# Optimization experiments

Hardware: AMD Instinct MI355X
Metric: run time of the kernel (lower is better)

The kernel has to match this reference:

```python
import jax, jax.numpy as jnp
import numpy as np

B, D_IN, H, D_OUT = 1024, 512, 512, 512


def _act(v):
    # torch.relu(x) ** 2
    r = jnp.maximum(v, 0.0)
    return r * r


def setup_inputs() -> dict:
    key = jax.random.key(0)
    ks = jax.random.split(key, 8)
    x = jax.random.normal(ks[0], (B, D_IN), dtype=jnp.float32)
    # input_to_hidden: Linear(D_IN, H)
    W_in = jax.random.normal(ks[1], (D_IN, H), dtype=jnp.float32) / np.sqrt(D_IN)
    b_in = jax.random.normal(ks[2], (H,), dtype=jnp.float32) * 0.01
    # hidden_to_hidden[i]: Linear(1, H-i-1). Pack into padded arrays [H-1, H]
    # where row i, column j is the weight feeding output index j (valid only j > i).
    W_hh = jax.random.normal(ks[3], (H - 1, H), dtype=jnp.float32) * 0.02
    b_hh = jax.random.normal(ks[4], (H - 1, H), dtype=jnp.float32) * 0.01
    # hidden_to_output: Linear(H, D_OUT)
    W_out = jax.random.normal(ks[5], (H, D_OUT), dtype=jnp.float32) / np.sqrt(H)
    b_out = jax.random.normal(ks[6], (D_OUT,), dtype=jnp.float32) * 0.01
    return {"x": x, "W_in": W_in, "b_in": b_in, "W_hh": W_hh, "b_hh": b_hh,
            "W_out": W_out, "b_out": b_out}


def reference(x, W_in, b_in, W_hh, b_hh, W_out, b_out):
    h0 = _act(x @ W_in + b_in)  # [B, H]
    hid = h0.shape[1]
    col = jnp.arange(hid)

    def step(h, inp):
        i, w, b = inp  # w, b: [H] padded rows
        src = jnp.take(h, i, axis=1)  # [B], uses UPDATED h (strict sequential dep)
        contrib = _act(src[:, None] * w[None, :] + b[None, :])  # [B, H]
        mask = (col > i).astype(h.dtype)  # only columns i+1.. get updated
        return h + contrib * mask[None, :], None

    xs = (jnp.arange(hid - 1), W_hh, b_hh)
    h, _ = jax.lax.scan(step, h0, xs)
    return h @ W_out + b_out  # [B, D_OUT]
```

## Files before the change

### kernel.cpp

```cpp
#include <hip/hip_runtime.h>

#define B_SZ 1024
#define DIN 512
#define HH 512
#define DOUT 512

typedef short bf16x8 __attribute__((ext_vector_type(8)));
typedef float f32x4 __attribute__((ext_vector_type(4)));

__device__ __forceinline__ unsigned short f2bf(float f) {
    unsigned int u = __float_as_uint(f);
    u += 0x7FFFu + ((u >> 16) & 1u);
    return (unsigned short)(u >> 16);
}
__device__ __forceinline__ float bf2f(unsigned short s) {
    return __uint_as_float(((unsigned int)s) << 16);
}

__device__ __forceinline__ uint4 cvt8(const float4& a0, const float4& a1, int term) {
    const float av[8] = {a0.x, a0.y, a0.z, a0.w, a1.x, a1.y, a1.z, a1.w};
    unsigned int p[4];
    #pragma unroll
    for (int q = 0; q < 4; ++q) {
        float f0 = av[2 * q], f1 = av[2 * q + 1];
        unsigned short h0 = f2bf(f0), h1 = f2bf(f1);
        if (term == 1) { h0 = f2bf(f0 - bf2f(h0)); h1 = f2bf(f1 - bf2f(h1)); }
        p[q] = (unsigned int)h0 | ((unsigned int)h1 << 16);
    }
    uint4 v; v.x = p[0]; v.y = p[1]; v.z = p[2]; v.w = p[3];
    return v;
}

__device__ __forceinline__ void gload_lds16(const void* g, void* l) {
    __builtin_amdgcn_global_load_lds(
        (__attribute__((address_space(1))) void*)g,
        (__attribute__((address_space(3))) void*)l, 16, 0, 0);
}

__device__ __forceinline__ void convW_body(const float* __restrict__ W,
                                           uint4* __restrict__ dst, int t) {
    const int lane = t & 63;
    const int fb   = t >> 6;
    const int ks   = fb >> 5;
    const int nf   = fb & 31;
    const int col  = nf * 16 + (lane & 15);
    const int kb   = ks * 32 + ((lane >> 4) << 3);
    const int term = kb >> 9;
    const int c0   = kb & 511;
    unsigned short o[8];
    #pragma unroll
    for (int j = 0; j < 8; ++j) {
        const float f = W[(size_t)(c0 + j) * 512 + col];
        unsigned short hi = f2bf(f);
        o[j] = (term == 2) ? f2bf(f - bf2f(hi)) : hi;
    }
    uint4 v;
    v.x = (unsigned int)o[0] | ((unsigned int)o[1] << 16);
    v.y = (unsigned int)o[2] | ((unsigned int)o[3] << 16);
    v.z = (unsigned int)o[4] | ((unsigned int)o[5] << 16);
    v.w = (unsigned int)o[6] | ((unsigned int)o[7] << 16);
    dst[t] = v;
}

template <int C>
__device__ __forceinline__ void pack_bulk(const float* __restrict__ W_hh,
                                          const float* __restrict__ b_hh,
                                          float2* __restrict__ wbk, int e) {
    constexpr int NK = 7 - C;
    constexpr int CB = (C==0?0:C==1?7:C==2?13:C==3?18:C==4?22:C==5?25:27) * 4096;
    const int s   = e / (NK * 64);
    const int rem = e - s * (NK * 64);
    const int row = 64 * C + s;
    const int col = 64 * (C + 1) + rem;
    float2 o;
    o.x = W_hh[(size_t)row * 512 + col];
    o.y = b_hh[(size_t)row * 512 + col];
    wbk[CB + e] = o;
}

__global__ __launch_bounds__(256)
void prep_all(const float* __restrict__ W_hh, const float* __restrict__ b_hh,
              float2* __restrict__ wdg, float2* __restrict__ wbk,
              const float* __restrict__ W_in, uint4* __restrict__ Bin,
              const float* __restrict__ W_out, uint4* __restrict__ Bout) {
    const int b = blockIdx.x;
    const int tid = threadIdx.x;
    if (b < 128) {
        const int idx = b * 256 + tid;
        const int i = idx >> 6, l = idx & 63;
        float2 o;
        if (i < 511 && l > (i & 63)) {
            const int col = ((i >> 6) << 6) + l;
            o.x = W_hh[(size_t)i * 512 + col];
            o.y = b_hh[(size_t)i * 512 + col];
        } else { o.x = 0.0f; o.y = -1.0f; }
        wdg[idx] = o;
    } else if (b < 576) {
        const int rb = b - 128;
        if      (rb < 112) pack_bulk<0>(W_hh, b_hh, wbk, (rb      ) * 256 + tid);
        else if (rb < 208) pack_bulk<1>(W_hh, b_hh, wbk, (rb - 112) * 256 + tid);
        else if (rb < 288) pack_bulk<2>(W_hh, b_hh, wbk, (rb - 208) * 256 + tid);
        else if (rb < 352) pack_bulk<3>(W_hh, b_hh, wbk, (rb - 288) * 256 + tid);
        else if (rb < 400) pack_bulk<4>(W_hh, b_hh, wbk, (rb - 352) * 256 + tid);
        else if (rb < 432) pack_bulk<5>(W_hh, b_hh, wbk, (rb - 400) * 256 + tid);
        else               pack_bulk<6>(W_hh, b_hh, wbk, (rb - 432) * 256 + tid);
    } else if (b < 960) {
        convW_body(W_in, Bin, (b - 576) * 256 + tid);
    } else {
        convW_body(W_out, Bout, (b - 960) * 256 + tid);
    }
}

template <bool ACT>
__global__ __launch_bounds__(512, 2)
void mfma_gemm(const float* __restrict__ A,
               const uint4* __restrict__ Bg,
               const float* __restrict__ bias,
               float* __restrict__ C) {
    __shared__ uint4 lds[2][768];
    const int tid  = threadIdx.x;
    const int lane = tid & 63;
    const int w    = tid >> 6;
    const int mfw  = w & 3;
    const int nfw  = w >> 2;
    const int mf0  = blockIdx.x * 4;
    const int nf0  = blockIdx.y * 2;

    const int ks_s = tid >> 8;
    const int mf_s = (tid >> 6) & 3;
    const int arow = (mf0 + mf_s) * 16 + (lane & 15);
    const int koff = (lane >> 4) << 3;
    const int bks  = tid >> 7;
    const int bnf  = (tid >> 6) & 1;

    float4 Ra0, Ra1; uint4 R2;
    auto stage = [&](int s) {
        const int kp = (s * 2 + ks_s) * 32 + koff;
        const int c  = kp & 511;
        Ra0 = *(const float4*)&A[(size_t)arow * 512 + c];
        Ra1 = *(const float4*)&A[(size_t)arow * 512 + c + 4];
        if (tid < 256)
            R2 = Bg[(size_t)((s * 2 + bks) * 32 + nf0 + bnf) * 64 + lane];
    };
    auto write_tile = [&](int buf, int s) {
        const int kp = (s * 2 + ks_s) * 32 + koff;
        lds[buf][ks_s * 256 + mf_s * 64 + lane] = cvt8(Ra0, Ra1, kp >> 9);
        if (tid < 256)
            lds[buf][512 + bks * 128 + bnf * 64 + lane] = R2;
    };

    f32x4 acc = {0.f, 0.f, 0.f, 0.f};

    stage(0);
    write_tile(0, 0);
    stage(1);
    __syncthreads();

    for (int s = 0; s < 24; ++s) {
        const int cur = s & 1;
        if (s + 1 < 24) write_tile(cur ^ 1, s + 1);
        if (s + 2 < 24) stage(s + 2);
        __builtin_amdgcn_sched_barrier(0);

        bf16x8 aF0 = *(const bf16x8*)&lds[cur][          mfw * 64 + lane];
        bf16x8 aF1 = *(const bf16x8*)&lds[cur][256     + mfw * 64 + lane];
        bf16x8 bF0 = *(const bf16x8*)&lds[cur][512     + nfw * 64 + lane];
        bf16x8 bF1 = *(const bf16x8*)&lds[cur][512+128 + nfw * 64 + lane];
        acc = __builtin_amdgcn_mfma_f32_16x16x32_bf16(aF0, bF0, acc, 0, 0, 0);
        acc = __builtin_amdgcn_mfma_f32_16x16x32_bf16(aF1, bF1, acc, 0, 0, 0);
        __syncthreads();
    }

    const int colg  = (nf0 + nfw) * 16 + (lane & 15);
    const float bv  = bias[colg];
    const int rbase = (mf0 + mfw) * 16 + ((lane >> 4) << 2);
    #pragma unroll
    for (int r = 0; r < 4; ++r) {
        float v = acc[r] + bv;
        if (ACT) { v = fmaxf(v, 0.f); v = v * v; }
        C[(size_t)(rbase + r) * 512 + colg] = v;
    }
}

template <int C>
__device__ __forceinline__ void scan_chunk(const float2* __restrict__ wdg,
                                           const float2* __restrict__ wbk,
                                           float2 (* __restrict__ smb)[3584],
                                           float hr[8], int lane, int tid) {
    constexpr int NK = 7 - C;
    constexpr int CB = (C==0?0:C==1?7:C==2?13:C==3?18:C==4?22:C==5?25:C==6?27:27) * 4096;
    const float2* dptr = wdg + (64 * C) * 64 + lane;

    float2 Wd[16];
    #pragma unroll
    for (int q = 0; q < 16; ++q) Wd[q] = dptr[q * 64];

    const char* gch = (const char*)(wbk + CB);
    char* lbase = (char*)(&smb[0][0]) + ((tid >> 6) << 10);
    auto stage = [&](int t, int buf) {
        const char* g = gch + (size_t)t * (NK * 4096);
        char* l = lbase + buf * 28672;
        #pragma unroll
        for (int u = 0; u < NK; ++u)
            gload_lds16(g + (size_t)((u << 8) + tid) * 16, l + (u << 12));
    };
    if constexpr (NK > 0) stage(0, 0);

    for (int t = 0; t < 4; ++t) {
        #pragma unroll
        for (int q = 0; q < 16; ++q) {
            const int s = t * 16 + q;
            if (!(C == 7 && s == 63)) {
                const float hi = __uint_as_float(
                    __builtin_amdgcn_readlane(__float_as_uint(hr[C]), s));
                const float tv = fmaf(hi, Wd[q].x, Wd[q].y);
                const float rv = fmaxf(tv, 0.f);
                hr[C] = fmaf(rv, rv, hr[C]);
            }
            if (t < 3) Wd[q] = dptr[(s + 16) * 64];
        }
    }

    if constexpr (NK > 0) {
        __syncthreads();
        for (int t = 0; t < 8; ++t) {
            const int buf = t & 1;
            if (t + 1 < 8) stage(t + 1, buf ^ 1);
            __builtin_amdgcn_sched_barrier(0);

            #pragma unroll 2
            for (int s = 0; s < 8; ++s) {
                const float hi = __uint_as_float(
                    __builtin_amdgcn_readlane(__float_as_uint(hr[C]), t * 8 + s));
                #pragma unroll
                for (int k = 0; k < NK; ++k) {
                    const float2 wv = smb[buf][(s * NK + k) * 64 + lane];
                    const float tv = fmaf(hi, wv.x, wv.y);
                    const float rv = fmaxf(tv, 0.f);
                    hr[C + 1 + k] = fmaf(rv, rv, hr[C + 1 + k]);
                }
            }
            __syncthreads();
        }
    }
}

__global__ __launch_bounds__(256, 1)
void scan_kernel(const float2* __restrict__ wdg, const float2* __restrict__ wbk,
                 float* __restrict__ h) {
    __shared__ __align__(16) float2 smb[2][3584];
    const int tid  = threadIdx.x;
    const int lane = tid & 63;
    const int wave = tid >> 6;
    const int row  = blockIdx.x * 4 + wave;
    float* hrow = h + (size_t)row * HH;

    float hr[8];
    #pragma unroll
    for (int k = 0; k < 8; ++k) hr[k] = hrow[lane + 64 * k];

    scan_chunk<0>(wdg, wbk, smb, hr, lane, tid);
    scan_chunk<1>(wdg, wbk, smb, hr, lane, tid);
    scan_chunk<2>(wdg, wbk, smb, hr, lane, tid);
    scan_chunk<3>(wdg, wbk, smb, hr, lane, tid);
    scan_chunk<4>(wdg, wbk, smb, hr, lane, tid);
    scan_chunk<5>(wdg, wbk, smb, hr, lane, tid);
    scan_chunk<6>(wdg, wbk, smb, hr, lane, tid);
    scan_chunk<7>(wdg, wbk, smb, hr, lane, tid);

    #pragma unroll
    for (int k = 0; k < 8; ++k) hrow[lane + 64 * k] = hr[k];
}

extern "C" void kernel_launch(void* const* d_in, const int* in_sizes, int n_in,
                              void* d_out, int out_size, void* d_ws, size_t ws_size,
                              hipStream_t stream) {
    const float* x     = (const float*)d_in[0];
    const float* W_in  = (const float*)d_in[1];
    const float* b_in  = (const float*)d_in[2];
    const float* W_hh  = (const float*)d_in[3];
    const float* b_hh  = (const float*)d_in[4];
    const float* W_out = (const float*)d_in[5];
    const float* b_out = (const float*)d_in[6];
    float* out = (float*)d_out;

    char* ws = (char*)d_ws;
    float2* wdg  = (float2*)ws;
    float2* wbk  = (float2*)(ws + 0x040000u);
    float*  h    = (float*)(ws + 0x120000u);
    uint4*  Bin  = (uint4*)(ws + 0x320000u);
    uint4*  Bout = (uint4*)(ws + 0x4A0000u);

    prep_all<<<dim3(1344), dim3(256), 0, stream>>>(W_hh, b_hh, wdg, wbk,
                                                   W_in, Bin, W_out, Bout);

    mfma_gemm<true><<<dim3(16, 16), dim3(512), 0, stream>>>(x, Bin, b_in, h);

    scan_kernel<<<dim3(256), dim3(256), 0, stream>>>(wdg, wbk, h);

    mfma_gemm<false><<<dim3(16, 16), dim3(512), 0, stream>>>(h, Bout, b_out, out);
}
```

Before: 157.1 us.

## Split each scan row across two waves with LDS partial-sum exchange

Each batch row is now handled by two waves instead of one, doubling the grid to 512 blocks with 2 rows per block. The waves split the off-diagonal source steps by parity and accumulate partial sums that are combined through shared memory before each diagonal chunk, which one wave still computes alone. Launch bounds are raised to allow two blocks per CU. This adds parallelism to the latency-bound sequential scan, at the cost of extra barriers, idle time for the second wave during the diagonal part, and twice the staged weight traffic per row.

```diff
diff --git a/kernel.cpp b/kernel.cpp
--- a/kernel.cpp
+++ b/kernel.cpp
@@ -186,14 +186,11 @@
 __device__ __forceinline__ void scan_chunk(const float2* __restrict__ wdg,
                                            const float2* __restrict__ wbk,
                                            float2 (* __restrict__ smb)[3584],
-                                           float hr[8], int lane, int tid) {
+                                           float (* __restrict__ comm)[64],
+                                           float hrp[8], int lane, int row_l,
+                                           int par, int tid) {
     constexpr int NK = 7 - C;
     constexpr int CB = (C==0?0:C==1?7:C==2?13:C==3?18:C==4?22:C==5?25:C==6?27:27) * 4096;
-    const float2* dptr = wdg + (64 * C) * 64 + lane;
-
-    float2 Wd[16];
-    #pragma unroll
-    for (int q = 0; q < 16; ++q) Wd[q] = dptr[q * 64];
 
     const char* gch = (const char*)(wbk + CB);
     char* lbase = (char*)(&smb[0][0]) + ((tid >> 6) << 10);
@@ -205,39 +202,53 @@
             gload_lds16(g + (size_t)((u << 8) + tid) * 16, l + (u << 12));
     };
     if constexpr (NK > 0) stage(0, 0);
-
-    for (int t = 0; t < 4; ++t) {
+    __builtin_amdgcn_sched_barrier(0);
+
+    if (par == 1) comm[row_l][lane] = hrp[C];
+    __syncthreads();
+
+    if (par == 0) {
+        hrp[C] += comm[row_l][lane];
+        const float2* dptr = wdg + (64 * C) * 64 + lane;
+        float2 Wd[16];
         #pragma unroll
-        for (int q = 0; q < 16; ++q) {
-            const int s = t * 16 + q;
-            if (!(C == 7 && s == 63)) {
-                const float hi = __uint_as_float(
-                    __builtin_amdgcn_readlane(__float_as_uint(hr[C]), s));
-                const float tv = fmaf(hi, Wd[q].x, Wd[q].y);
-                const float rv = fmaxf(tv, 0.f);
-                hr[C] = fmaf(rv, rv, hr[C]);
+        for (int q = 0; q < 16; ++q) Wd[q] = dptr[q * 64];
+        for (int t = 0; t < 4; ++t) {
+            #pragma unroll
+            for (int q = 0; q < 16; ++q) {
+                const int s = t * 16 + q;
+                if (!(C == 7 && s == 63)) {
+                    const float hi = __uint_as_float(
+                        __builtin_amdgcn_readlane(__float_as_uint(hrp[C]), s));
+                    const float tv = fmaf(hi, Wd[q].x, Wd[q].y);
+                    const float rv = fmaxf(tv, 0.f);
+                    hrp[C] = fmaf(rv, rv, hrp[C]);
+                }
+                if (t < 3) Wd[q] = dptr[(s + 16) * 64];
             }
-            if (t < 3) Wd[q] = dptr[(s + 16) * 64];
         }
-    }
+        comm[row_l][lane] = hrp[C];
+    }
+    __syncthreads();
 
     if constexpr (NK > 0) {
-        __syncthreads();
+        const float hsrc = (par == 0) ? hrp[C] : comm[row_l][lane];
         for (int t = 0; t < 8; ++t) {
             const int buf = t & 1;
             if (t + 1 < 8) stage(t + 1, buf ^ 1);
             __builtin_amdgcn_sched_barrier(0);
 
-            #pragma unroll 2
-            for (int s = 0; s < 8; ++s) {
+            #pragma unroll
+            for (int sl = 0; sl < 4; ++sl) {
+                const int srow = 2 * sl + par;
                 const float hi = __uint_as_float(
-                    __builtin_amdgcn_readlane(__float_as_uint(hr[C]), t * 8 + s));
+                    __builtin_amdgcn_readlane(__float_as_uint(hsrc), t * 8 + srow));
                 #pragma unroll
                 for (int k = 0; k < NK; ++k) {
-                    const float2 wv = smb[buf][(s * NK + k) * 64 + lane];
+                    const float2 wv = smb[buf][(srow * NK + k) * 64 + lane];
                     const float tv = fmaf(hi, wv.x, wv.y);
                     const float rv = fmaxf(tv, 0.f);
-                    hr[C + 1 + k] = fmaf(rv, rv, hr[C + 1 + k]);
+                    hrp[C + 1 + k] = fmaf(rv, rv, hrp[C + 1 + k]);
                 }
             }
             __syncthreads();
@@ -245,31 +256,35 @@
     }
 }
 
-__global__ __launch_bounds__(256, 1)
+__global__ __launch_bounds__(256, 2)
 void scan_kernel(const float2* __restrict__ wdg, const float2* __restrict__ wbk,
                  float* __restrict__ h) {
     __shared__ __align__(16) float2 smb[2][3584];
-    const int tid  = threadIdx.x;
-    const int lane = tid & 63;
-    const int wave = tid >> 6;
-    const int row  = blockIdx.x * 4 + wave;
-    float* hrow = h + (size_t)row * HH;
-
-    float hr[8];
+    __shared__ float comm[2][64];
+    const int tid   = threadIdx.x;
+    const int lane  = tid & 63;
+    const int w     = tid >> 6;
+    const int row_l = w & 1;
+    const int par   = w >> 1;
+    float* hrow = h + (size_t)(blockIdx.x * 2 + row_l) * HH;
+
+    float hrp[8];
     #pragma unroll
-    for (int k = 0; k < 8; ++k) hr[k] = hrow[lane + 64 * k];
-
-    scan_chunk<0>(wdg, wbk, smb, hr, lane, tid);
-    scan_chunk<1>(wdg, wbk, smb, hr, lane, tid);
-    scan_chunk<2>(wdg, wbk, smb, hr, lane, tid);
-    scan_chunk<3>(wdg, wbk, smb, hr, lane, tid);
-    scan_chunk<4>(wdg, wbk, smb, hr, lane, tid);
-    scan_chunk<5>(wdg, wbk, smb, hr, lane, tid);
-    scan_chunk<6>(wdg, wbk, smb, hr, lane, tid);
-    scan_chunk<7>(wdg, wbk, smb, hr, lane, tid);
-
-    #pragma unroll
-    for (int k = 0; k < 8; ++k) hrow[lane + 64 * k] = hr[k];
+    for (int k = 0; k < 8; ++k) hrp[k] = (par == 0) ? hrow[lane + 64 * k] : 0.f;
+
+    scan_chunk<0>(wdg, wbk, smb, comm, hrp, lane, row_l, par, tid);
+    scan_chunk<1>(wdg, wbk, smb, comm, hrp, lane, row_l, par, tid);
+    scan_chunk<2>(wdg, wbk, smb, comm, hrp, lane, row_l, par, tid);
+    scan_chunk<3>(wdg, wbk, smb, comm, hrp, lane, row_l, par, tid);
+    scan_chunk<4>(wdg, wbk, smb, comm, hrp, lane, row_l, par, tid);
+    scan_chunk<5>(wdg, wbk, smb, comm, hrp, lane, row_l, par, tid);
+    scan_chunk<6>(wdg, wbk, smb, comm, hrp, lane, row_l, par, tid);
+    scan_chunk<7>(wdg, wbk, smb, comm, hrp, lane, row_l, par, tid);
+
+    if (par == 0) {
+        #pragma unroll
+        for (int k = 0; k < 8; ++k) hrow[lane + 64 * k] = hrp[k];
+    }
 }
 
 extern "C" void kernel_launch(void* const* d_in, const int* in_sizes, int n_in,
@@ -296,7 +311,7 @@
 
     mfma_gemm<true><<<dim3(16, 16), dim3(512), 0, stream>>>(x, Bin, b_in, h);
 
-    scan_kernel<<<dim3(256), dim3(256), 0, stream>>>(wdg, wbk, h);
+    scan_kernel<<<dim3(512), dim3(256), 0, stream>>>(wdg, wbk, h);
 
     mfma_gemm<false><<<dim3(16, 16), dim3(512), 0, stream>>>(h, Bout, b_out, out);
 }
```

Measured after the change: 151.1 us. 3.8% less time.

## Split scan rows across waves with partial-sum reduction for more parallelism

Applied to the files above, without the earlier changes.

Changes the scan kernel from one batch row per wave to two rows per block, with each of the four waves handling a quarter of the source steps in the off-diagonal update and keeping partial sums. Before each diagonal chunk, the partial sums are reduced through shared memory, and the designated wave runs the serial diagonal recurrence. The grid is doubled to 512 blocks and launch bounds allow two blocks per CU. The aim is to shorten the per-row serial critical path and raise occupancy. In exchange it adds extra barriers, LDS traffic for the reductions, and idle waves during the diagonal phase.

```diff
diff --git a/kernel.cpp b/kernel.cpp
--- a/kernel.cpp
+++ b/kernel.cpp
@@ -36,6 +36,7 @@
         (__attribute__((address_space(1))) void*)g,
         (__attribute__((address_space(3))) void*)l, 16, 0, 0);
 }
+__device__ __forceinline__ void SB() { __builtin_amdgcn_sched_barrier(0); }
 
 __device__ __forceinline__ void convW_body(const float* __restrict__ W,
                                            uint4* __restrict__ dst, int t) {
@@ -186,14 +187,11 @@
 __device__ __forceinline__ void scan_chunk(const float2* __restrict__ wdg,
                                            const float2* __restrict__ wbk,
                                            float2 (* __restrict__ smb)[3584],
-                                           float hr[8], int lane, int tid) {
+                                           float (* __restrict__ comm)[4][64],
+                                           float hA[8], float hB[8],
+                                           int lane, int p, int tid) {
     constexpr int NK = 7 - C;
     constexpr int CB = (C==0?0:C==1?7:C==2?13:C==3?18:C==4?22:C==5?25:C==6?27:27) * 4096;
-    const float2* dptr = wdg + (64 * C) * 64 + lane;
-
-    float2 Wd[16];
-    #pragma unroll
-    for (int q = 0; q < 16; ++q) Wd[q] = dptr[q * 64];
 
     const char* gch = (const char*)(wbk + CB);
     char* lbase = (char*)(&smb[0][0]) + ((tid >> 6) << 10);
@@ -205,39 +203,68 @@
             gload_lds16(g + (size_t)((u << 8) + tid) * 16, l + (u << 12));
     };
     if constexpr (NK > 0) stage(0, 0);
-
-    for (int t = 0; t < 4; ++t) {
+    SB();
+
+    if (p != 0) comm[0][p][lane] = hA[C];
+    if (p != 1) comm[1][p][lane] = hB[C];
+    __syncthreads();
+
+    auto diag = [&](float& x) {
+        const float2* dptr = wdg + (64 * C) * 64 + lane;
+        float2 Wd[16];
         #pragma unroll
-        for (int q = 0; q < 16; ++q) {
-            const int s = t * 16 + q;
-            if (!(C == 7 && s == 63)) {
-                const float hi = __uint_as_float(
-                    __builtin_amdgcn_readlane(__float_as_uint(hr[C]), s));
-                const float tv = fmaf(hi, Wd[q].x, Wd[q].y);
-                const float rv = fmaxf(tv, 0.f);
-                hr[C] = fmaf(rv, rv, hr[C]);
+        for (int q = 0; q < 16; ++q) Wd[q] = dptr[q * 64];
+        for (int t = 0; t < 4; ++t) {
+            #pragma unroll
+            for (int q = 0; q < 16; ++q) {
+                const int s = t * 16 + q;
+                if (!(C == 7 && s == 63)) {
+                    const float hi = __uint_as_float(
+                        __builtin_amdgcn_readlane(__float_as_uint(x), s));
+                    const float tv = fmaf(hi, Wd[q].x, Wd[q].y);
+                    const float rv = fmaxf(tv, 0.f);
+                    x = fmaf(rv, rv, x);
+                }
+                if (t < 3) Wd[q] = dptr[(s + 16) * 64];
             }
-            if (t < 3) Wd[q] = dptr[(s + 16) * 64];
         }
-    }
+    };
+    if (p == 0) {
+        hA[C] += comm[0][1][lane] + comm[0][2][lane] + comm[0][3][lane];
+        diag(hA[C]);
+        comm[0][0][lane] = hA[C];
+    } else if (p == 1) {
+        hB[C] += comm[1][0][lane] + comm[1][2][lane] + comm[1][3][lane];
+        diag(hB[C]);
+        comm[1][1][lane] = hB[C];
+    }
+    __syncthreads();
 
     if constexpr (NK > 0) {
-        __syncthreads();
+        const float hsA = (p == 0) ? hA[C] : comm[0][0][lane];
+        const float hsB = (p == 1) ? hB[C] : comm[1][1][lane];
         for (int t = 0; t < 8; ++t) {
             const int buf = t & 1;
             if (t + 1 < 8) stage(t + 1, buf ^ 1);
-            __builtin_amdgcn_sched_barrier(0);
-
-            #pragma unroll 2
-            for (int s = 0; s < 8; ++s) {
-                const float hi = __uint_as_float(
-                    __builtin_amdgcn_readlane(__float_as_uint(hr[C]), t * 8 + s));
+            SB();
+
+            #pragma unroll
+            for (int sl = 0; sl < 2; ++sl) {
+                const int srow = p + 4 * sl;
+                const int s = t * 8 + srow;
+                const float hiA = __uint_as_float(
+                    __builtin_amdgcn_readlane(__float_as_uint(hsA), s));
+                const float hiB = __uint_as_float(
+                    __builtin_amdgcn_readlane(__float_as_uint(hsB), s));
                 #pragma unroll
                 for (int k = 0; k < NK; ++k) {
-                    const float2 wv = smb[buf][(s * NK + k) * 64 + lane];
-                    const float tv = fmaf(hi, wv.x, wv.y);
-                    const float rv = fmaxf(tv, 0.f);
-                    hr[C + 1 + k] = fmaf(rv, rv, hr[C + 1 + k]);
+                    const float2 wv = smb[buf][(srow * NK + k) * 64 + lane];
+                    float tv = fmaf(hiA, wv.x, wv.y);
+                    float rv = fmaxf(tv, 0.f);
+                    hA[C + 1 + k] = fmaf(rv, rv, hA[C + 1 + k]);
+                    tv = fmaf(hiB, wv.x, wv.y);
+                    rv = fmaxf(tv, 0.f);
+                    hB[C + 1 + k] = fmaf(rv, rv, hB[C + 1 + k]);
                 }
             }
             __syncthreads();
@@ -245,31 +272,40 @@
     }
 }
 
-__global__ __launch_bounds__(256, 1)
+__global__ __launch_bounds__(256, 2)
 void scan_kernel(const float2* __restrict__ wdg, const float2* __restrict__ wbk,
                  float* __restrict__ h) {
     __shared__ __align__(16) float2 smb[2][3584];
+    __shared__ float comm[2][4][64];
     const int tid  = threadIdx.x;
     const int lane = tid & 63;
-    const int wave = tid >> 6;
-    const int row  = blockIdx.x * 4 + wave;
-    float* hrow = h + (size_t)row * HH;
-
-    float hr[8];
+    const int p    = tid >> 6;
+    float* hrowA = h + (size_t)(blockIdx.x * 2    ) * HH;
+    float* hrowB = h + (size_t)(blockIdx.x * 2 + 1) * HH;
+
+    float hA[8], hB[8];
     #pragma unroll
-    for (int k = 0; k < 8; ++k) hr[k] = hrow[lane + 64 * k];
-
-    scan_chunk<0>(wdg, wbk, smb, hr, lane, tid);
-    scan_chunk<1>(wdg, wbk, smb, hr, lane, tid);
-    scan_chunk<2>(wdg, wbk, smb, hr, lane, tid);
-    scan_chunk<3>(wdg, wbk, smb, hr, lane, tid);
-    scan_chunk<4>(wdg, wbk, smb, hr, lane, tid);
-    scan_chunk<5>(wdg, wbk, smb, hr, lane, tid);
-    scan_chunk<6>(wdg, wbk, smb, hr, lane, tid);
-    scan_chunk<7>(wdg, wbk, smb, hr, lane, tid);
-
-    #pragma unroll
-    for (int k = 0; k < 8; ++k) hrow[lane + 64 * k] = hr[k];
+    for (int k = 0; k < 8; ++k) {
+        hA[k] = (p == 0) ? hrowA[lane + 64 * k] : 0.f;
+        hB[k] = (p == 1) ? hrowB[lane + 64 * k] : 0.f;
+    }
+
+    scan_chunk<0>(wdg, wbk, smb, comm, hA, hB, lane, p, tid);
+    scan_chunk<1>(wdg, wbk, smb, comm, hA, hB, lane, p, tid);
+    scan_chunk<2>(wdg, wbk, smb, comm, hA, hB, lane, p, tid);
+    scan_chunk<3>(wdg, wbk, smb, comm, hA, hB, lane, p, tid);
+    scan_chunk<4>(wdg, wbk, smb, comm, hA, hB, lane, p, tid);
+    scan_chunk<5>(wdg, wbk, smb, comm, hA, hB, lane, p, tid);
+    scan_chunk<6>(wdg, wbk, smb, comm, hA, hB, lane, p, tid);
+    scan_chunk<7>(wdg, wbk, smb, comm, hA, hB, lane, p, tid);
+
+    if (p == 0) {
+        #pragma unroll
+        for (int k = 0; k < 8; ++k) hrowA[lane + 64 * k] = hA[k];
+    } else if (p == 1) {
+        #pragma unroll
+        for (int k = 0; k < 8; ++k) hrowB[lane + 64 * k] = hB[k];
+    }
 }
 
 extern "C" void kernel_launch(void* const* d_in, const int* in_sizes, int n_in,
@@ -296,7 +332,7 @@
 
     mfma_gemm<true><<<dim3(16, 16), dim3(512), 0, stream>>>(x, Bin, b_in, h);
 
-    scan_kernel<<<dim3(256), dim3(256), 0, stream>>>(wdg, wbk, h);
+    scan_kernel<<<dim3(512), dim3(256), 0, stream>>>(wdg, wbk, h);
 
     mfma_gemm<false><<<dim3(16, 16), dim3(512), 0, stream>>>(h, Bout, b_out, out);
 }
```

New measurement: 149.6 us (median of 3 runs). 4.8% less time.

## Split scan off-diagonal updates across 8 waves with LDS partial-sum reduction

Applied to the files above, without the earlier changes.

The scan kernel now runs 512 threads per block. The 8 waves split each chunk's off-diagonal step range, and every wave keeps partial hidden-state sums for all 4 rows. Before each chunk's sequential diagonal part, the partials are reduced through a shared comm buffer, one owning wave runs the diagonal, and the result is broadcast back through LDS. This doubles the parallelism per row for the dominant off-diagonal work, at the cost of extra LDS traffic, more barriers, and more registers per thread.

```diff
diff --git a/kernel.cpp b/kernel.cpp
--- a/kernel.cpp
+++ b/kernel.cpp
@@ -36,6 +36,7 @@
         (__attribute__((address_space(1))) void*)g,
         (__attribute__((address_space(3))) void*)l, 16, 0, 0);
 }
+__device__ __forceinline__ void SB() { __builtin_amdgcn_sched_barrier(0); }
 
 __device__ __forceinline__ void convW_body(const float* __restrict__ W,
                                            uint4* __restrict__ dst, int t) {
@@ -186,14 +187,11 @@
 __device__ __forceinline__ void scan_chunk(const float2* __restrict__ wdg,
                                            const float2* __restrict__ wbk,
                                            float2 (* __restrict__ smb)[3584],
-                                           float hr[8], int lane, int tid) {
+                                           float (* __restrict__ comm)[8][64],
+                                           float hR[4][8], int lane, int p,
+                                           int tid) {
     constexpr int NK = 7 - C;
     constexpr int CB = (C==0?0:C==1?7:C==2?13:C==3?18:C==4?22:C==5?25:C==6?27:27) * 4096;
-    const float2* dptr = wdg + (64 * C) * 64 + lane;
-
-    float2 Wd[16];
-    #pragma unroll
-    for (int q = 0; q < 16; ++q) Wd[q] = dptr[q * 64];
 
     const char* gch = (const char*)(wbk + CB);
     char* lbase = (char*)(&smb[0][0]) + ((tid >> 6) << 10);
@@ -204,40 +202,67 @@
         for (int u = 0; u < NK; ++u)
             gload_lds16(g + (size_t)((u << 8) + tid) * 16, l + (u << 12));
     };
-    if constexpr (NK > 0) stage(0, 0);
-
-    for (int t = 0; t < 4; ++t) {
+    if constexpr (NK > 0) { if (tid < 256) stage(0, 0); }
+    SB();
+
+    #pragma unroll
+    for (int r = 0; r < 4; ++r) comm[r][p][lane] = hR[r][C];
+    __syncthreads();
+
+    #pragma unroll
+    for (int r = 0; r < 4; ++r) {
+        if (p == r) {
+            float x = 0.f;
+            #pragma unroll
+            for (int q = 0; q < 8; ++q) x += comm[r][q][lane];
+            const float2* dptr = wdg + (64 * C) * 64 + lane;
+            float2 Wd[16];
+            #pragma unroll
+            for (int q = 0; q < 16; ++q) Wd[q] = dptr[q * 64];
+            for (int t = 0; t < 4; ++t) {
+                #pragma unroll
+                for (int q = 0; q < 16; ++q) {
+                    const int s = t * 16 + q;
+                    if (!(C == 7 && s == 63)) {
+                        const float hi = __uint_as_float(
+                            __builtin_amdgcn_readlane(__float_as_uint(x), s));
+                        const float tv = fmaf(hi, Wd[q].x, Wd[q].y);
+                        const float rv = fmaxf(tv, 0.f);
+                        x = fmaf(rv, rv, x);
+                    }
+                    if (t < 3) Wd[q] = dptr[(s + 16) * 64];
+                }
+            }
+            hR[r][C] = x;
+            comm[r][r][lane] = x;
+        }
+    }
+    __syncthreads();
+
+    if constexpr (NK > 0) {
+        float hs[4];
         #pragma unroll
-        for (int q = 0; q < 16; ++q) {
-            const int s = t * 16 + q;
-            if (!(C == 7 && s == 63)) {
-                const float hi = __uint_as_float(
-                    __builtin_amdgcn_readlane(__float_as_uint(hr[C]), s));
-                const float tv = fmaf(hi, Wd[q].x, Wd[q].y);
-                const float rv = fmaxf(tv, 0.f);
-                hr[C] = fmaf(rv, rv, hr[C]);
-            }
-            if (t < 3) Wd[q] = dptr[(s + 16) * 64];
-        }
-    }
-
-    if constexpr (NK > 0) {
-        __syncthreads();
+        for (int r = 0; r < 4; ++r)
+            hs[r] = (p == r) ? hR[r][C] : comm[r][r][lane];
         for (int t = 0; t < 8; ++t) {
             const int buf = t & 1;
-            if (t + 1 < 8) stage(t + 1, buf ^ 1);
-            __builtin_amdgcn_sched_barrier(0);
-
-            #pragma unroll 2
-            for (int s = 0; s < 8; ++s) {
-                const float hi = __uint_as_float(
-                    __builtin_amdgcn_readlane(__float_as_uint(hr[C]), t * 8 + s));
+            if (tid < 256 && t + 1 < 8) stage(t + 1, buf ^ 1);
+            SB();
+
+            const int s = t * 8 + p;
+            float hi[4];
+            #pragma unroll
+            for (int r = 0; r < 4; ++r)
+                hi[r] = __uint_as_float(
+                    __builtin_amdgcn_readlane(__float_as_uint(hs[r]), s));
+            #pragma unroll
+            for (int k = 0; k < NK; ++k) {
+                const float2 wv = smb[buf][(p * NK + k) * 64 + lane];
                 #pragma unroll
-                for (int k = 0; k < NK; ++k) {
-                    const float2 wv = smb[buf][(s * NK + k) * 64 + lane];
-                    const float tv = fmaf(hi, wv.x, wv.y);
+                for (int r = 0; r < 4; ++r) {
+                    const float tv = fmaf(hi[r], wv.x, wv.y);
                     const float rv = fmaxf(tv, 0.f);
-                    hr[C + 1 + k] = fmaf(rv, rv, hr[C + 1 + k]);
+                    hR[r][C + 1 + k] = fmaf(rv, rv, hR[r][C + 1 + k]);
                 }
             }
             __syncthreads();
@@ -245,31 +270,41 @@
     }
 }
 
-__global__ __launch_bounds__(256, 1)
+__global__ __launch_bounds__(512, 2)
 void scan_kernel(const float2* __restrict__ wdg, const float2* __restrict__ wbk,
                  float* __restrict__ h) {
     __shared__ __align__(16) float2 smb[2][3584];
+    __shared__ float comm[4][8][64];
     const int tid  = threadIdx.x;
     const int lane = tid & 63;
-    const int wave = tid >> 6;
-    const int row  = blockIdx.x * 4 + wave;
-    float* hrow = h + (size_t)row * HH;
-
-    float hr[8];
-    #pragma unroll
-    for (int k = 0; k < 8; ++k) hr[k] = hrow[lane + 64 * k];
-
-    scan_chunk<0>(wdg, wbk, smb, hr, lane, tid);
-    scan_chunk<1>(wdg, wbk, smb, hr, lane, tid);
-    scan_chunk<2>(wdg, wbk, smb, hr, lane, tid);
-    scan_chunk<3>(wdg, wbk, smb, hr, lane, tid);
-    scan_chunk<4>(wdg, wbk, smb, hr, lane, tid);
-    scan_chunk<5>(wdg, wbk, smb, hr, lane, tid);
-    scan_chunk<6>(wdg, wbk, smb, hr, lane, tid);
-    scan_chunk<7>(wdg, wbk, smb, hr, lane, tid);
-
-    #pragma unroll
-    for (int k = 0; k < 8; ++k) hrow[lane + 64 * k] = hr[k];
+    const int p    = tid >> 6;
+
+    float hR[4][8];
+    #pragma unroll
+    for (int r = 0; r < 4; ++r) {
+        const float* hrow = h + (size_t)(blockIdx.x * 4 + r) * HH;
+        #pragma unroll
+        for (int k = 0; k < 8; ++k)
+            hR[r][k] = (p == r) ? hrow[lane + 64 * k] : 0.f;
+    }
+
+    scan_chunk<0>(wdg, wbk, smb, comm, hR, lane, p, tid);
+    scan_chunk<1>(wdg, wbk, smb, comm, hR, lane, p, tid);
+    scan_chunk<2>(wdg, wbk, smb, comm, hR, lane, p, tid);
+    scan_chunk<3>(wdg, wbk, smb, comm, hR, lane, p, tid);
+    scan_chunk<4>(wdg, wbk, smb, comm, hR, lane, p, tid);
+    scan_chunk<5>(wdg, wbk, smb, comm, hR, lane, p, tid);
+    scan_chunk<6>(wdg, wbk, smb, comm, hR, lane, p, tid);
+    scan_chunk<7>(wdg, wbk, smb, comm, hR, lane, p, tid);
+
+    #pragma unroll
+    for (int r = 0; r < 4; ++r) {
+        if (p == r) {
+            float* hrow = h + (size_t)(blockIdx.x * 4 + r) * HH;
+            #pragma unroll
+            for (int k = 0; k < 8; ++k) hrow[lane + 64 * k] = hR[r][k];
+        }
+    }
 }
 
 extern "C" void kernel_launch(void* const* d_in, const int* in_sizes, int n_in,
@@ -296,7 +331,7 @@
 
     mfma_gemm<true><<<dim3(16, 16), dim3(512), 0, stream>>>(x, Bin, b_in, h);
 
-    scan_kernel<<<dim3(256), dim3(256), 0, stream>>>(wdg, wbk, h);
+    scan_kernel<<<dim3(256), dim3(512), 0, stream>>>(wdg, wbk, h);
 
     mfma_gemm<false><<<dim3(16, 16), dim3(512), 0, stream>>>(h, Bout, b_out, out);
 }
```

Measured after the change: 161.0 us. 2.5% more time.
